# Optimization experiments

Hardware: AMD Instinct MI355X
Metric: run time of the kernel (lower is better)

The kernel has to match this reference:

```python
import jax, jax.numpy as jnp
import numpy as np

N_EXPERTS = 8
TOP_K = 2


def setup_inputs() -> dict:
    key = jax.random.key(0)
    ks = jax.random.split(key, 5)
    B, T, C, E, H = 8, 2048, 256, 8, 682  # H = int(8/3*256)
    scale = 1.0 / np.sqrt(C)
    return {
        "x": jax.random.normal(ks[0], (B, T, C), dtype=jnp.float32),
        "router_w": jax.random.normal(ks[1], (E, C), dtype=jnp.float32) * scale,
        "w1": jax.random.normal(ks[2], (E, H, C), dtype=jnp.float32) * scale,
        "w2": jax.random.normal(ks[3], (E, C, H), dtype=jnp.float32) * (1.0 / np.sqrt(H)),
        "w3": jax.random.normal(ks[4], (E, H, C), dtype=jnp.float32) * scale,
    }


def reference(x, router_w, w1, w2, w3):
    B, T, C = x.shape
    flat = x.reshape(-1, C)  # [N, C]

    # Router: softmax over experts, top-k selection, renormalize.
    logits = flat @ router_w.T                     # [N, E]
    probs = jax.nn.softmax(logits, axis=-1)
    topk_probs, topk_idx = jax.lax.top_k(probs, TOP_K)
    topk_probs = topk_probs / (jnp.sum(topk_probs, axis=-1, keepdims=True) + 1e-9)

    # Dense gate matrix [N, E]: zero for non-selected experts (same math as
    # the masked loop, since unselected experts contribute weight 0).
    onehot = jax.nn.one_hot(topk_idx, N_EXPERTS, dtype=flat.dtype)  # [N, K, E]
    gates = jnp.einsum("nk,nke->ne", topk_probs, onehot)           # [N, E]

    # SwiGLU experts, computed densely over E and combined with gates.
    h1 = jnp.einsum("nc,ehc->neh", flat, w1)       # [N, E, H]
    h3 = jnp.einsum("nc,ehc->neh", flat, w3)       # [N, E, H]
    h = jax.nn.silu(h1) * h3                       # [N, E, H]
    y = jnp.einsum("neh,ech->nec", h, w2)          # [N, E, C]
    out = jnp.einsum("ne,nec->nc", gates, y)       # [N, C]
    return out.reshape(B, T, C)
```

## Files before the change

### kernel.cpp

```cpp
#include <hip/hip_runtime.h>
#include <hip/hip_bf16.h>

#define N_TOK 16384
#define C_DIM 256
#define E_NUM 8
#define H_DIM 682
#define H_PAD 768
#define NROWS (N_TOK * 2)
#define HB 64
#define APB (NROWS / HB)

typedef short short8 __attribute__((ext_vector_type(8)));
typedef float floatx4 __attribute__((ext_vector_type(4)));
typedef unsigned int uint;

__device__ inline unsigned short f2bf(float v) {
    union { float f; uint u; } x; x.f = v;
    uint r = (x.u + 0x7fffu + ((x.u >> 16) & 1u)) >> 16;
    return (unsigned short)r;
}
__device__ inline float bf2f(unsigned short v) {
    union { uint u; float f; } x; x.u = ((uint)v) << 16; return x.f;
}

__device__ __forceinline__ void load_lds16(const void* g, void* l) {
    __builtin_amdgcn_global_load_lds(
        (const __attribute__((address_space(1))) unsigned int*)g,
        (__attribute__((address_space(3))) unsigned int*)l, 16, 0, 0);
}

#define VMCNT8 asm volatile("s_waitcnt vmcnt(8)" ::: "memory")
#define VMCNT6 asm volatile("s_waitcnt vmcnt(6)" ::: "memory")
#define VMCNT0 asm volatile("s_waitcnt vmcnt(0)" ::: "memory")
#define LGKM0  asm volatile("s_waitcnt lgkmcnt(0)" ::: "memory")

#define P13 (E_NUM * H_PAD * (C_DIM / 2))
#define P2  (E_NUM * C_DIM * (H_PAD / 2))
#define WCONV_BLKS ((2 * P13 + P2) / 256)

__global__ __launch_bounds__(256) void prep_kernel(
    const float* __restrict__ w1, const float* __restrict__ w3, const float* __restrict__ w2,
    unsigned short* __restrict__ w1b, unsigned short* __restrict__ w3b,
    unsigned short* __restrict__ w2b,
    const float* __restrict__ x, const float* __restrict__ rw,
    unsigned short* __restrict__ xb, int* __restrict__ as_e, float* __restrict__ as_gate) {
    __shared__ float rws[E_NUM * C_DIM];
    int tid = threadIdx.x;
    if (blockIdx.x < WCONV_BLKS) {
        int idx = blockIdx.x * 256 + tid;
        if (idx < 2 * P13) {
            const float* src = (idx < P13) ? w1 : w3;
            unsigned short* dst = (idx < P13) ? w1b : w3b;
            int i = (idx < P13) ? idx : idx - P13;
            int e = i / (H_PAD * (C_DIM / 2));
            int rem = i - e * (H_PAD * (C_DIM / 2));
            int r = rem / (C_DIM / 2);
            int c2 = rem - r * (C_DIM / 2);
            uint v = 0;
            if (r < H_DIM) {
                const float2 f = *(const float2*)(src + ((size_t)e * H_DIM + r) * C_DIM + c2 * 2);
                v = (uint)f2bf(f.x) | ((uint)f2bf(f.y) << 16);
            }
            ((uint*)dst)[i] = v;
        } else {
            int i = idx - 2 * P13;
            int e = i / (C_DIM * (H_PAD / 2));
            int rem = i - e * (C_DIM * (H_PAD / 2));
            int r = rem / (H_PAD / 2);
            int c2 = rem - r * (H_PAD / 2);
            uint v = 0;
            if (c2 * 2 < H_DIM) {
                const float2 f = *(const float2*)(w2 + ((size_t)e * C_DIM + r) * H_DIM + c2 * 2);
                v = (uint)f2bf(f.x) | ((uint)f2bf(f.y) << 16);
            }
            ((uint*)w2b)[i] = v;
        }
        return;
    }
    for (int i = tid; i < E_NUM * C_DIM; i += 256) rws[i] = rw[i];
    __syncthreads();
    int wave = tid >> 6, lane = tid & 63;
    int t = (blockIdx.x - WCONV_BLKS) * 4 + wave;
    const float4 xv = *(const float4*)(x + (size_t)t * C_DIM + lane * 4);
    uint2 pk;
    pk.x = (uint)f2bf(xv.x) | ((uint)f2bf(xv.y) << 16);
    pk.y = (uint)f2bf(xv.z) | ((uint)f2bf(xv.w) << 16);
    *(uint2*)(xb + (size_t)t * C_DIM + lane * 4) = pk;
    float p[E_NUM];
#pragma unroll
    for (int e = 0; e < E_NUM; e++) {
        const float* wr = &rws[e * C_DIM + lane * 4];
        p[e] = xv.x * wr[0] + xv.y * wr[1] + xv.z * wr[2] + xv.w * wr[3];
    }
#pragma unroll
    for (int off = 32; off >= 1; off >>= 1) {
#pragma unroll
        for (int e = 0; e < E_NUM; e++) p[e] += __shfl_down(p[e], off, 64);
    }
    if (lane == 0) {
        float m = p[0];
#pragma unroll
        for (int e = 1; e < E_NUM; e++) m = fmaxf(m, p[e]);
        float s = 0.f, q[E_NUM];
#pragma unroll
        for (int e = 0; e < E_NUM; e++) { q[e] = expf(p[e] - m); s += q[e]; }
#pragma unroll
        for (int e = 0; e < E_NUM; e++) q[e] /= s;
        int e0 = 0;
#pragma unroll
        for (int e = 1; e < E_NUM; e++) if (q[e] > q[e0]) e0 = e;
        int e1 = (e0 == 0) ? 1 : 0;
#pragma unroll
        for (int e = 0; e < E_NUM; e++) {
            if (e != e0 && q[e] > q[e1]) e1 = e;
        }
        float g0 = q[e0], g1 = q[e1];
        float denom = g0 + g1 + 1e-9f;
        g0 /= denom; g1 /= denom;
        as_e[t * 2] = e0; as_gate[t * 2] = g0;
        as_e[t * 2 + 1] = e1; as_gate[t * 2 + 1] = g1;
    }
}

__global__ __launch_bounds__(256) void hist_kernel(const int* __restrict__ as_e,
                                                   int* __restrict__ block_hist) {
    __shared__ int lh[E_NUM];
    int b = blockIdx.x, tid = threadIdx.x;
    if (tid < E_NUM) lh[tid] = 0;
    __syncthreads();
    for (int i = tid; i < APB; i += 256) atomicAdd(&lh[as_e[b * APB + i]], 1);
    __syncthreads();
    if (tid < E_NUM) block_hist[b * E_NUM + tid] = lh[tid];
}

__global__ void scan2_kernel(const int* __restrict__ block_hist, int* __restrict__ offsets,
                             int* __restrict__ block_base) {
    __shared__ int tot[E_NUM], off[E_NUM];
    int e = threadIdx.x;
    if (e < E_NUM) {
        int s = 0;
        for (int b = 0; b < HB; b++) s += block_hist[b * E_NUM + e];
        tot[e] = s;
    }
    __syncthreads();
    if (e == 0) {
        int acc = 0;
        for (int i = 0; i < E_NUM; i++) { off[i] = acc; offsets[i] = acc; acc += tot[i]; }
        offsets[E_NUM] = acc;
    }
    __syncthreads();
    if (e < E_NUM) {
        int acc = off[e];
        for (int b = 0; b < HB; b++) { block_base[b * E_NUM + e] = acc; acc += block_hist[b * E_NUM + e]; }
    }
}

__global__ __launch_bounds__(256) void scatter_kernel(
    const int* __restrict__ as_e, const int* __restrict__ block_base,
    int* __restrict__ row_token, int* __restrict__ as_row) {
    __shared__ int cur[E_NUM];
    int b = blockIdx.x, tid = threadIdx.x;
    if (tid < E_NUM) cur[tid] = block_base[b * E_NUM + tid];
    __syncthreads();
    for (int i = tid; i < APB; i += 256) {
        int a = b * APB + i;
        int e = as_e[a];
        int p = atomicAdd(&cur[e], 1);
        row_token[p] = a >> 1;
        as_row[a] = p;
    }
}

__global__ __launch_bounds__(256, 2) void expert_ffn1(
    const unsigned short* __restrict__ xb, const unsigned short* __restrict__ w1b,
    const unsigned short* __restrict__ w3b, const int* __restrict__ offsets,
    const int* __restrict__ row_token, unsigned short* __restrict__ h) {
    int e = blockIdx.x >> 6;
    int mt = blockIdx.x & 63;
    int c = blockIdx.y;
    int off0 = offsets[e], off1 = offsets[e + 1];
    int row0 = off0 + mt * 128;
    if (row0 >= off1) return;
    int mval = min(128, off1 - row0);

    __shared__ union {
        unsigned short buf[3][12288];
        unsigned short Hs[128 * 136];
    } sm;

    int tid = threadIdx.x, lane = tid & 63, w = tid >> 6;
    int wm = w & 1, wn = w >> 1;
    int ra = tid >> 2;
    int acol = (((tid & 3) ^ ((ra >> 1) & 3))) * 8;
    int tok0 = row_token[row0 + min(ra, mval - 1)];
    int tok1 = row_token[row0 + min(ra + 64, mval - 1)];
    const unsigned short* a0p = xb + (size_t)tok0 * C_DIM + acol;
    const unsigned short* a1p = xb + (size_t)tok1 * C_DIM + acol;
    const unsigned short* b1p0 = w1b + ((size_t)e * H_PAD + c * 128 + ra) * C_DIM + acol;
    const unsigned short* b1p1 = b1p0 + (size_t)64 * C_DIM;
    const unsigned short* b3p0 = w3b + ((size_t)e * H_PAD + c * 128 + ra) * C_DIM + acol;
    const unsigned short* b3p1 = b3p0 + (size_t)64 * C_DIM;

    int wofs = w * 512;
    auto stage = [&](int kt, unsigned short* base) {
        int kb = kt * 32;
        load_lds16(a0p + kb, base + wofs);
        load_lds16(a1p + kb, base + 2048 + wofs);
        load_lds16(b1p0 + kb, base + 4096 + wofs);
        load_lds16(b1p1 + kb, base + 6144 + wofs);
        load_lds16(b3p0 + kb, base + 8192 + wofs);
        load_lds16(b3p1 + kb, base + 10240 + wofs);
    };

    int ko = ((lane >> 4) ^ ((lane >> 1) & 3)) * 8;
    int l15 = lane & 15;
    int arowf = wm * 64 + l15;
    int browf = wn * 64 + l15;
    int quad = lane >> 4;

    stage(0, sm.buf[0]);
    stage(1, sm.buf[1]);

    floatx4 acc1[4][4], acc3[4][4];
#pragma unroll
    for (int m = 0; m < 4; m++)
#pragma unroll
        for (int n = 0; n < 4; n++) {
            acc1[m][n] = (floatx4){0.f, 0.f, 0.f, 0.f};
            acc3[m][n] = (floatx4){0.f, 0.f, 0.f, 0.f};
        }

#pragma unroll
    for (int kt = 0; kt < 8; kt++) {
        if (kt == 7) { VMCNT0; } else { VMCNT6; }
        __builtin_amdgcn_s_barrier();
        if (kt + 2 < 8) stage(kt + 2, sm.buf[(kt + 2) % 3]);
        const unsigned short* cur = sm.buf[kt % 3];
        short8 af[4], b1f[4], b3f[4];
#pragma unroll
        for (int m = 0; m < 4; m++) af[m] = *(short8*)&cur[(arowf + m * 16) * 32 + ko];
#pragma unroll
        for (int n = 0; n < 4; n++) {
            b1f[n] = *(short8*)&cur[4096 + (browf + n * 16) * 32 + ko];
            b3f[n] = *(short8*)&cur[8192 + (browf + n * 16) * 32 + ko];
        }
        __builtin_amdgcn_s_setprio(1);
#pragma unroll
        for (int m = 0; m < 4; m++)
#pragma unroll
            for (int n = 0; n < 4; n++) {
                acc1[m][n] = __builtin_amdgcn_mfma_f32_16x16x32_bf16(af[m], b1f[n], acc1[m][n], 0, 0, 0);
                acc3[m][n] = __builtin_amdgcn_mfma_f32_16x16x32_bf16(af[m], b3f[n], acc3[m][n], 0, 0, 0);
            }
        __builtin_amdgcn_s_setprio(0);
        __builtin_amdgcn_s_barrier();
    }
    __syncthreads();

#pragma unroll
    for (int m = 0; m < 4; m++)
#pragma unroll
        for (int n = 0; n < 4; n++)
#pragma unroll
            for (int r = 0; r < 4; r++) {
                float h1 = acc1[m][n][r], h3 = acc3[m][n][r];
                float sv = h1 / (1.0f + __expf(-h1)) * h3;
                sm.Hs[(wm * 64 + m * 16 + quad * 4 + r) * 136 + wn * 64 + n * 16 + l15] = f2bf(sv);
            }
    __syncthreads();
#pragma unroll
    for (int it = 0; it < 8; it++) {
        int s = it * 256 + tid;
        int row = s >> 4, c16 = s & 15;
        if (row < mval)
            *(int4*)(h + (size_t)(row0 + row) * H_PAD + c * 128 + c16 * 8) =
                *(int4*)&sm.Hs[row * 136 + c16 * 8];
    }
}

__global__ __launch_bounds__(256, 2) void expert_ffn2(
    const unsigned short* __restrict__ h, const unsigned short* __restrict__ w2b,
    const int* __restrict__ offsets, unsigned short* __restrict__ y) {
    int e = blockIdx.x >> 6;
    int mt = blockIdx.x & 63;
    int p = blockIdx.y;
    int off0 = offsets[e], off1 = offsets[e + 1];
    int row0 = off0 + mt * 128;
    if (row0 >= off1) return;
    int mval = min(128, off1 - row0);

    __shared__ union {
        unsigned short buf[2][16384];
        unsigned short Hs[128 * 136];
    } sm;

    int tid = threadIdx.x, lane = tid & 63, w = tid >> 6;
    int wm = w & 1, wn = w >> 1;
    int ra = tid >> 2;
    int acol = (((tid & 3) ^ ((ra >> 1) & 3))) * 8;
    const unsigned short* ap0 = h + (size_t)(row0 + ra) * H_PAD + acol;
    const unsigned short* ap1 = ap0 + (size_t)64 * H_PAD;
    const unsigned short* bp0 = w2b + ((size_t)e * C_DIM + p * 128 + ra) * H_PAD + acol;
    const unsigned short* bp1 = bp0 + (size_t)64 * H_PAD;

    int wofs = w * 512;
    auto stage = [&](int kt, unsigned short* base) {
        int kb = kt * 64;
#pragma unroll
        for (int kk = 0; kk < 2; kk++) {
            int ks = kb + kk * 32;
            unsigned short* b2 = base + kk * 8192;
            load_lds16(ap0 + ks, b2 + wofs);
            load_lds16(ap1 + ks, b2 + 2048 + wofs);
            load_lds16(bp0 + ks, b2 + 4096 + wofs);
            load_lds16(bp1 + ks, b2 + 6144 + wofs);
        }
    };

    int ko = ((lane >> 4) ^ ((lane >> 1) & 3)) * 8;
    int l15 = lane & 15;
    int arowf = wm * 64 + l15;
    int browf = wn * 64 + l15;
    int quad = lane >> 4;

    stage(0, sm.buf[0]);

    floatx4 acc[4][4];
#pragma unroll
    for (int m = 0; m < 4; m++)
#pragma unroll
        for (int n = 0; n < 4; n++) acc[m][n] = (floatx4){0.f, 0.f, 0.f, 0.f};

#pragma unroll
    for (int kt = 0; kt < H_PAD / 64; kt++) {
        if (kt + 1 < H_PAD / 64) stage(kt + 1, sm.buf[(kt + 1) & 1]);
        if (kt + 1 < H_PAD / 64) { VMCNT8; } else { VMCNT0; }
        __builtin_amdgcn_s_barrier();
        const unsigned short* cur = sm.buf[kt & 1];
#pragma unroll
        for (int kk = 0; kk < 2; kk++) {
            const unsigned short* c2 = cur + kk * 8192;
            short8 af[4], bf[4];
#pragma unroll
            for (int m = 0; m < 4; m++) af[m] = *(short8*)&c2[(arowf + m * 16) * 32 + ko];
#pragma unroll
            for (int n = 0; n < 4; n++) bf[n] = *(short8*)&c2[4096 + (browf + n * 16) * 32 + ko];
            __builtin_amdgcn_s_setprio(1);
#pragma unroll
            for (int m = 0; m < 4; m++)
#pragma unroll
                for (int n = 0; n < 4; n++)
                    acc[m][n] = __builtin_amdgcn_mfma_f32_16x16x32_bf16(af[m], bf[n], acc[m][n], 0, 0, 0);
            __builtin_amdgcn_s_setprio(0);
        }
        LGKM0;
        __builtin_amdgcn_s_barrier();
    }
    __syncthreads();

#pragma unroll
    for (int m = 0; m < 4; m++)
#pragma unroll
        for (int n = 0; n < 4; n++)
#pragma unroll
            for (int r = 0; r < 4; r++)
                sm.Hs[(wm * 64 + m * 16 + quad * 4 + r) * 136 + wn * 64 + n * 16 + l15] =
                    f2bf(acc[m][n][r]);
    __syncthreads();
#pragma unroll
    for (int it = 0; it < 8; it++) {
        int s = it * 256 + tid;
        int row = s >> 4, c16 = s & 15;
        if (row < mval)
            *(int4*)(y + (size_t)(row0 + row) * C_DIM + p * 128 + c16 * 8) =
                *(int4*)&sm.Hs[row * 136 + c16 * 8];
    }
}

__global__ __launch_bounds__(256) void combine_kernel(
    const unsigned short* __restrict__ y, const int* __restrict__ as_row,
    const float* __restrict__ as_gate, float* __restrict__ out) {
    int tid = threadIdx.x, lane = tid & 63;
    int t = blockIdx.x * 4 + (tid >> 6);
    int r0 = as_row[2 * t], r1 = as_row[2 * t + 1];
    float g0 = as_gate[2 * t], g1 = as_gate[2 * t + 1];
    uint2 a = *(const uint2*)(y + (size_t)r0 * C_DIM + lane * 4);
    uint2 b = *(const uint2*)(y + (size_t)r1 * C_DIM + lane * 4);
    float4 o;
    o.x = g0 * bf2f((unsigned short)(a.x & 0xffff)) + g1 * bf2f((unsigned short)(b.x & 0xffff));
    o.y = g0 * bf2f((unsigned short)(a.x >> 16)) + g1 * bf2f((unsigned short)(b.x >> 16));
    o.z = g0 * bf2f((unsigned short)(a.y & 0xffff)) + g1 * bf2f((unsigned short)(b.y & 0xffff));
    o.w = g0 * bf2f((unsigned short)(a.y >> 16)) + g1 * bf2f((unsigned short)(b.y >> 16));
    *(float4*)(out + (size_t)t * C_DIM + lane * 4) = o;
}

extern "C" void kernel_launch(void* const* d_in, const int* in_sizes, int n_in,
                              void* d_out, int out_size, void* d_ws, size_t ws_size,
                              hipStream_t stream) {
    const float* x = (const float*)d_in[0];
    const float* rw = (const float*)d_in[1];
    const float* w1 = (const float*)d_in[2];
    const float* w2 = (const float*)d_in[3];
    const float* w3 = (const float*)d_in[4];
    float* out = (float*)d_out;

    char* ws = (char*)d_ws;
    size_t o = 0;
    auto alloc = [&](size_t bytes) {
        void* p = ws + o;
        o = (o + bytes + 255) & ~(size_t)255;
        return p;
    };
    unsigned short* xb = (unsigned short*)alloc((size_t)N_TOK * C_DIM * 2);
    unsigned short* w1b = (unsigned short*)alloc((size_t)E_NUM * H_PAD * C_DIM * 2);
    unsigned short* w3b = (unsigned short*)alloc((size_t)E_NUM * H_PAD * C_DIM * 2);
    unsigned short* w2b = (unsigned short*)alloc((size_t)E_NUM * C_DIM * H_PAD * 2);
    unsigned short* hbuf = (unsigned short*)alloc((size_t)(NROWS + 128) * H_PAD * 2);
    unsigned short* ybuf = (unsigned short*)alloc((size_t)NROWS * C_DIM * 2);
    int* offsets = (int*)alloc((E_NUM + 1) * 4);
    int* as_e = (int*)alloc(NROWS * 4);
    float* as_gate = (float*)alloc(NROWS * 4);
    int* row_token = (int*)alloc(NROWS * 4);
    int* as_row = (int*)alloc(NROWS * 4);
    int* block_hist = (int*)alloc(HB * E_NUM * 4);
    int* block_base = (int*)alloc(HB * E_NUM * 4);

    prep_kernel<<<WCONV_BLKS + N_TOK / 4, 256, 0, stream>>>(
        w1, w3, w2, w1b, w3b, w2b, x, rw, xb, as_e, as_gate);
    hist_kernel<<<HB, 256, 0, stream>>>(as_e, block_hist);
    scan2_kernel<<<1, 64, 0, stream>>>(block_hist, offsets, block_base);
    scatter_kernel<<<HB, 256, 0, stream>>>(as_e, block_base, row_token, as_row);

    expert_ffn1<<<dim3(E_NUM * 64, 6), 256, 0, stream>>>(xb, w1b, w3b, offsets, row_token, hbuf);
    expert_ffn2<<<dim3(E_NUM * 64, 2), 256, 0, stream>>>(hbuf, w2b, offsets, ybuf);
    combine_kernel<<<N_TOK / 4, 256, 0, stream>>>(ybuf, as_row, as_gate, out);
}
```

Baseline: 194.8 us.

## Compact expert tile grid via prefix tile bases and use double-buffered LDS in ffn1

Adds a per-expert tile prefix sum in the scan kernel so the FFN kernels launch a compact grid of MAXTILE row tiles and map each block to its expert with a short search. This replaces the sparse 8x64 grid in which most blocks exited early. Separately, ffn1's LDS pipeline drops from triple to double buffering with an explicit LGKM wait, cutting shared memory per block at the cost of less load/compute overlap. MAXTILE must cover the worst-case tile count; 264 equals 256 full tiles plus one partial tile per expert, so the bound holds.

```diff
diff --git a/kernel.cpp b/kernel.cpp
--- a/kernel.cpp
+++ b/kernel.cpp
@@ -9,6 +9,7 @@
 #define NROWS (N_TOK * 2)
 #define HB 64
 #define APB (NROWS / HB)
+#define MAXTILE 264
 
 typedef short short8 __attribute__((ext_vector_type(8)));
 typedef float floatx4 __attribute__((ext_vector_type(4)));
@@ -134,7 +135,7 @@
 }
 
 __global__ void scan2_kernel(const int* __restrict__ block_hist, int* __restrict__ offsets,
-                             int* __restrict__ block_base) {
+                             int* __restrict__ block_base, int* __restrict__ tile_base) {
     __shared__ int tot[E_NUM], off[E_NUM];
     int e = threadIdx.x;
     if (e < E_NUM) {
@@ -147,6 +148,9 @@
         int acc = 0;
         for (int i = 0; i < E_NUM; i++) { off[i] = acc; offsets[i] = acc; acc += tot[i]; }
         offsets[E_NUM] = acc;
+        int t = 0;
+        tile_base[0] = 0;
+        for (int i = 0; i < E_NUM; i++) { t += (tot[i] + 127) / 128; tile_base[i + 1] = t; }
     }
     __syncthreads();
     if (e < E_NUM) {
@@ -171,20 +175,29 @@
     }
 }
 
+__device__ __forceinline__ int tile_to_expert(const int* __restrict__ tile_base, int bid) {
+    int e = 0;
+#pragma unroll
+    for (int i = 1; i < E_NUM; i++) e += (bid >= tile_base[i]) ? 1 : 0;
+    return e;
+}
+
 __global__ __launch_bounds__(256, 2) void expert_ffn1(
     const unsigned short* __restrict__ xb, const unsigned short* __restrict__ w1b,
     const unsigned short* __restrict__ w3b, const int* __restrict__ offsets,
-    const int* __restrict__ row_token, unsigned short* __restrict__ h) {
-    int e = blockIdx.x >> 6;
-    int mt = blockIdx.x & 63;
+    const int* __restrict__ tile_base, const int* __restrict__ row_token,
+    unsigned short* __restrict__ h) {
+    int bid = blockIdx.x;
+    if (bid >= tile_base[E_NUM]) return;
+    int e = tile_to_expert(tile_base, bid);
+    int mt = bid - tile_base[e];
     int c = blockIdx.y;
     int off0 = offsets[e], off1 = offsets[e + 1];
     int row0 = off0 + mt * 128;
-    if (row0 >= off1) return;
     int mval = min(128, off1 - row0);
 
     __shared__ union {
-        unsigned short buf[3][12288];
+        unsigned short buf[2][12288];
         unsigned short Hs[128 * 136];
     } sm;
 
@@ -219,7 +232,6 @@
     int quad = lane >> 4;
 
     stage(0, sm.buf[0]);
-    stage(1, sm.buf[1]);
 
     floatx4 acc1[4][4], acc3[4][4];
 #pragma unroll
@@ -232,10 +244,10 @@
 
 #pragma unroll
     for (int kt = 0; kt < 8; kt++) {
-        if (kt == 7) { VMCNT0; } else { VMCNT6; }
+        if (kt + 1 < 8) stage(kt + 1, sm.buf[(kt + 1) & 1]);
+        if (kt + 1 < 8) { VMCNT6; } else { VMCNT0; }
         __builtin_amdgcn_s_barrier();
-        if (kt + 2 < 8) stage(kt + 2, sm.buf[(kt + 2) % 3]);
-        const unsigned short* cur = sm.buf[kt % 3];
+        const unsigned short* cur = sm.buf[kt & 1];
         short8 af[4], b1f[4], b3f[4];
 #pragma unroll
         for (int m = 0; m < 4; m++) af[m] = *(short8*)&cur[(arowf + m * 16) * 32 + ko];
@@ -253,6 +265,7 @@
                 acc3[m][n] = __builtin_amdgcn_mfma_f32_16x16x32_bf16(af[m], b3f[n], acc3[m][n], 0, 0, 0);
             }
         __builtin_amdgcn_s_setprio(0);
+        LGKM0;
         __builtin_amdgcn_s_barrier();
     }
     __syncthreads();
@@ -280,13 +293,15 @@
 
 __global__ __launch_bounds__(256, 2) void expert_ffn2(
     const unsigned short* __restrict__ h, const unsigned short* __restrict__ w2b,
-    const int* __restrict__ offsets, unsigned short* __restrict__ y) {
-    int e = blockIdx.x >> 6;
-    int mt = blockIdx.x & 63;
+    const int* __restrict__ offsets, const int* __restrict__ tile_base,
+    unsigned short* __restrict__ y) {
+    int bid = blockIdx.x;
+    if (bid >= tile_base[E_NUM]) return;
+    int e = tile_to_expert(tile_base, bid);
+    int mt = bid - tile_base[e];
     int p = blockIdx.y;
     int off0 = offsets[e], off1 = offsets[e + 1];
     int row0 = off0 + mt * 128;
-    if (row0 >= off1) return;
     int mval = min(128, off1 - row0);
 
     __shared__ union {
@@ -418,6 +433,7 @@
     unsigned short* hbuf = (unsigned short*)alloc((size_t)(NROWS + 128) * H_PAD * 2);
     unsigned short* ybuf = (unsigned short*)alloc((size_t)NROWS * C_DIM * 2);
     int* offsets = (int*)alloc((E_NUM + 1) * 4);
+    int* tile_base = (int*)alloc((E_NUM + 1) * 4);
     int* as_e = (int*)alloc(NROWS * 4);
     float* as_gate = (float*)alloc(NROWS * 4);
     int* row_token = (int*)alloc(NROWS * 4);
@@ -428,10 +444,11 @@
     prep_kernel<<<WCONV_BLKS + N_TOK / 4, 256, 0, stream>>>(
         w1, w3, w2, w1b, w3b, w2b, x, rw, xb, as_e, as_gate);
     hist_kernel<<<HB, 256, 0, stream>>>(as_e, block_hist);
-    scan2_kernel<<<1, 64, 0, stream>>>(block_hist, offsets, block_base);
+    scan2_kernel<<<1, 64, 0, stream>>>(block_hist, offsets, block_base, tile_base);
     scatter_kernel<<<HB, 256, 0, stream>>>(as_e, block_base, row_token, as_row);
 
-    expert_ffn1<<<dim3(E_NUM * 64, 6), 256, 0, stream>>>(xb, w1b, w3b, offsets, row_token, hbuf);
-    expert_ffn2<<<dim3(E_NUM * 64, 2), 256, 0, stream>>>(hbuf, w2b, offsets, ybuf);
+    expert_ffn1<<<dim3(MAXTILE, 6), 256, 0, stream>>>(xb, w1b, w3b, offsets, tile_base,
+                                                      row_token, hbuf);
+    expert_ffn2<<<dim3(MAXTILE, 2), 256, 0, stream>>>(hbuf, w2b, offsets, tile_base, ybuf);
     combine_kernel<<<N_TOK / 4, 256, 0, stream>>>(ybuf, as_row, as_gate, out);
 }
```

Result: faster. 187.6 us (-3.7%).
